# Kernel optimization log

Hardware: AMD Instinct MI355X
Metric: run time of the kernel (lower is better)

The kernel has to match this reference:

```python
import jax, jax.numpy as jnp
import numpy as np

SCALES = (1, 3, 6)
PRECISION = 10  # pywt default: 2**10 samples of psi on [-5, 5]


def _gaus1_filters():
    """Replicates pywt.cwt's integrated-wavelet filters for wavelet='gaus1'.

    pywt: psi, x = wavelet.wavefun(10); int_psi = cumsum(psi)*step; per scale a:
    j = arange(a*(x[-1]-x[0])+1)/(a*step) -> int indices; filter = int_psi[j][::-1];
    conv = np.convolve(data, filter). np.convolve flips its kernel, so the
    equivalent cross-correlation kernel (lax.conv semantics) is int_psi[j].
    """
    x = np.linspace(-5.0, 5.0, 2 ** PRECISION)
    step = x[1] - x[0]
    psi = -2.0 * x * np.exp(-x ** 2) / (np.pi / 2.0) ** 0.25
    int_psi = np.cumsum(psi) * step
    filts = []
    for a in SCALES:
        j = (np.arange(a * (x[-1] - x[0]) + 1) / (a * step)).astype(np.int64)
        j = j[j < int_psi.size]
        filts.append(int_psi[j].astype(np.float32))  # correlation kernel
    return filts

_FILTS = _gaus1_filters()


def setup_inputs() -> dict:
    key = jax.random.key(0)
    x = jax.random.normal(key, (32, 4096, 64), dtype=jnp.float32)
    return {"x": x}


def reference(x):
    B, S, C = x.shape
    sig = jnp.transpose(x, (0, 2, 1)).reshape(B * C, 1, S)  # [B*C, 1, S]
    outs = []
    for a, f in zip(SCALES, _FILTS):
        L = f.shape[0]
        k = jnp.asarray(f).reshape(1, 1, L)
        # full convolution (np.convolve): pad L-1 both sides
        conv = jax.lax.conv_general_dilated(
            sig, k, window_strides=(1,), padding=[(L - 1, L - 1)],
            dimension_numbers=("NCH", "OIH", "NCH"))  # [B*C, 1, S+L-1]
        coef = -np.sqrt(a).astype(np.float32) * jnp.diff(conv, axis=-1)  # [B*C,1,S+L-2]
        d = (coef.shape[-1] - S) / 2.0
        coef = coef[..., int(np.floor(d)): coef.shape[-1] - int(np.ceil(d))]  # [B*C,1,S]
        outs.append(coef)
    out = jnp.concatenate(outs, axis=1).reshape(B, C, len(SCALES), S)
    return jnp.transpose(out, (0, 2, 3, 1))  # [B, 3, S, C]
```

## Files before the change

### kernel.cpp

```cpp
#include <hip/hip_runtime.h>
#include <math.h>

#define S_LEN  4096
#define NCH    64
#define TILE_S 64
#define RPT    8
#define TY     8
#define NROWS  128
#define WLEN   70


constexpr double cexp_(double v) {
  const double LN2 = 0.6931471805599453;
  double t = v / LN2;
  int k = (int)t;
  if (t < 0.0 && (double)k != t) --k;
  double r = v - (double)k * LN2;
  double term = 1.0, sum = 1.0;
  for (int n = 1; n <= 22; ++n) { term *= r / (double)n; sum += term; }
  while (k > 0) { sum *= 2.0; --k; }
  while (k < 0) { sum *= 0.5; ++k; }
  return sum;
}
constexpr double csqrt_(double a) {
  double y = a > 1.0 ? a : 1.0;
  for (int i = 0; i < 64; ++i) y = 0.5 * (y + a / y);
  return y;
}
struct Wt { float w6[62]; float w3[32]; float w1[12]; };
constexpr Wt make_weights() {
  Wt w{};
  double ip[1024] = {};
  const double delta = 10.0 / 1023.0;
  const double step  = (-5.0 + delta) + 5.0;
  const double cn    = csqrt_(csqrt_(1.5707963267948966));
  double s = 0.0;
  for (int i = 0; i < 1024; ++i) {
    const double xi  = (i == 1023) ? 5.0 : ((double)i * delta - 5.0);
    const double psi = (-2.0 * xi) * cexp_(-(xi * xi)) / cn;
    s += psi;
    ip[i] = s * step;
  }
  const int as_[3] = {6, 3, 1};
  const int lf_[3] = {61, 31, 11};
  for (int si = 0; si < 3; ++si) {
    const double denom = (double)as_[si] * step;
    const float  sqa   = (float)csqrt_((double)as_[si]);
    const int    lf    = lf_[si];
    for (int t = 0; t <= lf; ++t) {
      float km1 = 0.f, kt = 0.f;
      if (t >= 1)      km1 = (float)ip[(long)(((double)(t - 1)) / denom)];
      if (t <= lf - 1) kt  = (float)ip[(long)(((double)t) / denom)];
      const float val = -sqa * (km1 - kt);
      if (si == 0) w.w6[t] = val; else if (si == 1) w.w3[t] = val; else w.w1[t] = val;
    }
  }
  return w;
}
constexpr Wt CW = make_weights();
template <int T> constexpr float W6 = CW.w6[T];
template <int T> constexpr float W3 = CW.w3[T];
template <int T> constexpr float W1 = CW.w1[T];

template <int K>
struct PreW {
  static __device__ __forceinline__ void run(const float* __restrict__ colbase,
                                             float (&win)[WLEN]) {
    win[K] = colbase[K * NCH];
    PreW<K + 1>::run(colbase, win);
  }
};
template <>
struct PreW<63> {
  static __device__ __forceinline__ void run(const float* __restrict__, float (&)[WLEN]) {}
};

template <int R, int T>
struct Tap {
  static __device__ __forceinline__ void run(const float (&win)[WLEN], float& a6,
                                             float& a3, float& a1) {
    a6 = fmaf(W6<T>, win[T + R + 1], a6);
    if constexpr (T >= 15 && T <= 46) a3 = fmaf(W3<T - 15>, win[T + R + 1], a3);
    if constexpr (T >= 25 && T <= 36) a1 = fmaf(W1<T - 25>, win[T + R + 1], a1);
    Tap<R, T + 1>::run(win, a6, a3, a1);
  }
};
template <int R>
struct Tap<R, 62> {
  static __device__ __forceinline__ void run(const float (&)[WLEN], float&, float&, float&) {}
};

template <int R>
struct Row {
  static __device__ __forceinline__ void run(const float* __restrict__ colbase,
                                             float (&win)[WLEN], float* __restrict__ o1,
                                             float* __restrict__ o3, float* __restrict__ o6) {
    if constexpr (R > 0) win[R + 62] = colbase[(R + 62) * NCH];
    float a6 = 0.f, a3 = 0.f, a1 = 0.f;
    Tap<R, 0>::run(win, a6, a3, a1);
    o1[(size_t)R * NCH] = a1;
    o3[(size_t)R * NCH] = a3;
    o6[(size_t)R * NCH] = a6;
    Row<R + 1>::run(colbase, win, o1, o3, o6);
  }
};
template <>
struct Row<RPT> {
  static __device__ __forceinline__ void run(const float* __restrict__, float (&)[WLEN],
                                             float* __restrict__, float* __restrict__,
                                             float* __restrict__) {}
};

__global__ __launch_bounds__(512, 6)
void cwt_main(const float* __restrict__ x, float* __restrict__ out) {
  __shared__ __align__(16) float lds[NROWS * NCH];

  const int c  = threadIdx.x;
  const int ty = threadIdx.y;
  const int tid = ty * 64 + c;

  const int hw = blockIdx.x;
  const int wg = ((hw & 7) << 8) + (hw >> 3);
  const int sx = wg & 63;
  const int b  = wg >> 6;
  const int s0 = sx * TILE_S;
  const int ROW0 = s0 - 32;

  const float* __restrict__ xb = x + (size_t)b * S_LEN * NCH;

  #pragma unroll
  for (int i = 0; i < 4; ++i) {
    const int slot = tid + i * 512;
    const int row  = slot >> 4, q = slot & 15;
    const int grow = ROW0 + row;
    float4 v = make_float4(0.f, 0.f, 0.f, 0.f);
    if ((unsigned)grow < (unsigned)S_LEN)
      v = *(const float4*)(xb + ((size_t)grow * NCH + (q << 2)));
    *(float4*)&lds[row * NCH + (q << 2)] = v;
  }
  __syncthreads();

  const float* __restrict__ colbase = &lds[(RPT * ty) * NCH + c];

  float win[WLEN];
  PreW<1>::run(colbase, win);

  const int srow = s0 + RPT * ty;
  float* o1 = out + (((size_t)b * 3 + 0) * S_LEN + srow) * NCH + c;
  float* o3 = out + (((size_t)b * 3 + 1) * S_LEN + srow) * NCH + c;
  float* o6 = out + (((size_t)b * 3 + 2) * S_LEN + srow) * NCH + c;

  Row<0>::run(colbase, win, o1, o3, o6);
}

extern "C" void kernel_launch(void* const* d_in, const int* in_sizes, int n_in,
                              void* d_out, int out_size, void* d_ws, size_t ws_size,
                              hipStream_t stream) {
  (void)n_in; (void)out_size; (void)d_ws; (void)ws_size;
  const float* x = (const float*)d_in[0];
  float* out = (float*)d_out;
  const int B = in_sizes[0] / (S_LEN * NCH);

  const int nblk = (S_LEN / TILE_S) * B;
  dim3 grid(nblk);
  dim3 block(NCH, TY);
  hipLaunchKernelGGL(cwt_main, grid, block, 0, stream, x, out);
}
```

Before: 136.1 us.

## Recast convolution as banded-Toeplitz MFMA with split-bf16 inputs

Replaces the per-thread scalar FMA sliding-window convolution with matrix-core MFMA 16x16x32 bf16 operations. The constant Toeplitz weight tiles are prebuilt in constant memory. Each input is split into high and low bf16 halves so two MFMAs roughly recover fp32 accuracy, and these are staged transposed per channel in XOR-swizzled LDS. The tile per block grows to 128 rows. This is meant to remove the large FMA instruction count, at the cost of bf16 weight rounding error, reduced occupancy and strided scalar global loads.

After: 133.4 us. 2.0% less time.

```diff
diff --git a/kernel.cpp b/kernel.cpp
--- a/kernel.cpp
+++ b/kernel.cpp
@@ -3,11 +3,14 @@
 
 #define S_LEN  4096
 #define NCH    64
-#define TILE_S 64
-#define RPT    8
+#define BTILE  128
 #define TY     8
-#define NROWS  128
-#define WLEN   70
+#define NCHUNK 26
+#define CSTR   256
+
+typedef __attribute__((ext_vector_type(8)))  short   short8v;
+typedef __attribute__((ext_vector_type(8)))  __bf16  bf16x8;
+typedef __attribute__((ext_vector_type(4)))  float   f32x4;
 
 
 constexpr double cexp_(double v) {
@@ -57,100 +60,123 @@
   }
   return w;
 }
-constexpr Wt CW = make_weights();
-template <int T> constexpr float W6 = CW.w6[T];
-template <int T> constexpr float W3 = CW.w3[T];
-template <int T> constexpr float W1 = CW.w1[T];
 
-template <int K>
-struct PreW {
-  static __device__ __forceinline__ void run(const float* __restrict__ colbase,
-                                             float (&win)[WLEN]) {
-    win[K] = colbase[K * NCH];
-    PreW<K + 1>::run(colbase, win);
-  }
-};
-template <>
-struct PreW<63> {
-  static __device__ __forceinline__ void run(const float* __restrict__, float (&)[WLEN]) {}
-};
+constexpr unsigned short bf16rne(float f) {
+  const unsigned u = __builtin_bit_cast(unsigned, f);
+  return (unsigned short)((u + 0x7FFFu + ((u >> 16) & 1u)) >> 16);
+}
 
-template <int R, int T>
-struct Tap {
-  static __device__ __forceinline__ void run(const float (&win)[WLEN], float& a6,
-                                             float& a3, float& a1) {
-    a6 = fmaf(W6<T>, win[T + R + 1], a6);
-    if constexpr (T >= 15 && T <= 46) a3 = fmaf(W3<T - 15>, win[T + R + 1], a3);
-    if constexpr (T >= 25 && T <= 36) a1 = fmaf(W1<T - 25>, win[T + R + 1], a1);
-    Tap<R, T + 1>::run(win, a6, a3, a1);
-  }
-};
-template <int R>
-struct Tap<R, 62> {
-  static __device__ __forceinline__ void run(const float (&)[WLEN], float&, float&, float&) {}
-};
+struct __align__(16) ATab { unsigned short v[6][64][8]; };
+constexpr ATab make_atab() {
+  ATab t{};
+  constexpr Wt w = make_weights();
+  for (int f = 0; f < 6; ++f)
+    for (int l = 0; l < 64; ++l)
+      for (int e = 0; e < 8; ++e) {
+        const int i = l & 15, k = (l >> 4) * 8 + e;
+        float val = 0.f;
+        if (f < 3)      { const int d = 32 * f + k - i - 1;       if (d >= 0 && d < 62) val = w.w6[d]; }
+        else if (f < 5) { const int d = 32 * (f - 3) + k - i;     if (d >= 0 && d < 32) val = w.w3[d]; }
+        else            { const int d = k - i - 2;                if (d >= 0 && d < 12) val = w.w1[d]; }
+        t.v[f][l][e] = bf16rne(val);
+      }
+  return t;
+}
+__constant__ ATab g_at = make_atab();
 
-template <int R>
-struct Row {
-  static __device__ __forceinline__ void run(const float* __restrict__ colbase,
-                                             float (&win)[WLEN], float* __restrict__ o1,
-                                             float* __restrict__ o3, float* __restrict__ o6) {
-    if constexpr (R > 0) win[R + 62] = colbase[(R + 62) * NCH];
-    float a6 = 0.f, a3 = 0.f, a1 = 0.f;
-    Tap<R, 0>::run(win, a6, a3, a1);
-    o1[(size_t)R * NCH] = a1;
-    o3[(size_t)R * NCH] = a3;
-    o6[(size_t)R * NCH] = a6;
-    Row<R + 1>::run(colbase, win, o1, o3, o6);
-  }
-};
-template <>
-struct Row<RPT> {
-  static __device__ __forceinline__ void run(const float* __restrict__, float (&)[WLEN],
-                                             float* __restrict__, float* __restrict__,
-                                             float* __restrict__) {}
-};
-
-__global__ __launch_bounds__(512, 6)
+__global__ __launch_bounds__(512, 4)
 void cwt_main(const float* __restrict__ x, float* __restrict__ out) {
-  __shared__ __align__(16) float lds[NROWS * NCH];
+  __shared__ __align__(16) unsigned short lds[2][NCH * CSTR];
 
   const int c  = threadIdx.x;
   const int ty = threadIdx.y;
-  const int tid = ty * 64 + c;
 
-  const int hw = blockIdx.x;
-  const int wg = ((hw & 7) << 8) + (hw >> 3);
-  const int sx = wg & 63;
-  const int b  = wg >> 6;
-  const int s0 = sx * TILE_S;
-  const int ROW0 = s0 - 32;
+  const int hw  = blockIdx.x;
+  const int npx = gridDim.x >> 3;
+  const int wg  = (hw & 7) * npx + (hw >> 3);
+  const int sg  = wg & ((S_LEN / BTILE) - 1);
+  const int b   = wg / (S_LEN / BTILE);
+  const int BS0 = sg * BTILE;
+  const int ROW0 = BS0 - 32;
 
   const float* __restrict__ xb = x + (size_t)b * S_LEN * NCH;
 
   #pragma unroll
-  for (int i = 0; i < 4; ++i) {
-    const int slot = tid + i * 512;
-    const int row  = slot >> 4, q = slot & 15;
-    const int grow = ROW0 + row;
-    float4 v = make_float4(0.f, 0.f, 0.f, 0.f);
-    if ((unsigned)grow < (unsigned)S_LEN)
-      v = *(const float4*)(xb + ((size_t)grow * NCH + (q << 2)));
-    *(float4*)&lds[row * NCH + (q << 2)] = v;
+  for (int q = 0; q < 4; ++q) {
+    const int cidx = ty + 8 * q;
+    if (cidx < NCHUNK) {
+      const int r0 = ROW0 + cidx * 8;
+      float v[8];
+      #pragma unroll
+      for (int r = 0; r < 8; ++r) {
+        const int row = r0 + r;
+        v[r] = ((unsigned)row < (unsigned)S_LEN) ? xb[(size_t)row * NCH + c] : 0.f;
+      }
+      short8v ph, pl;
+      #pragma unroll
+      for (int r = 0; r < 8; ++r) {
+        const unsigned u  = __builtin_bit_cast(unsigned, v[r]);
+        const unsigned h  = (u + 0x7FFFu + ((u >> 16) & 1u)) >> 16;
+        const float    fh = __builtin_bit_cast(float, h << 16);
+        const float    rl = v[r] - fh;
+        const unsigned ul = __builtin_bit_cast(unsigned, rl);
+        const unsigned lo = (ul + 0x7FFFu + ((ul >> 16) & 1u)) >> 16;
+        ph[r] = (short)h; pl[r] = (short)lo;
+      }
+      const int base = c * CSTR + ((cidx ^ (c & 7)) << 3);
+      *(short8v*)&lds[0][base] = ph;
+      *(short8v*)&lds[1][base] = pl;
+    }
   }
   __syncthreads();
 
-  const float* __restrict__ colbase = &lds[(RPT * ty) * NCH + c];
+  const int j  = c & 15;
+  const int ck = c >> 4;
+  const int hh = c & 7;
 
-  float win[WLEN];
-  PreW<1>::run(colbase, win);
+  const bf16x8 A60 = *(const bf16x8*)&g_at.v[0][c][0];
+  const bf16x8 A61 = *(const bf16x8*)&g_at.v[1][c][0];
+  const bf16x8 A62 = *(const bf16x8*)&g_at.v[2][c][0];
+  const bf16x8 A30 = *(const bf16x8*)&g_at.v[3][c][0];
+  const bf16x8 A31 = *(const bf16x8*)&g_at.v[4][c][0];
+  const bf16x8 A10 = *(const bf16x8*)&g_at.v[5][c][0];
 
-  const int srow = s0 + RPT * ty;
-  float* o1 = out + (((size_t)b * 3 + 0) * S_LEN + srow) * NCH + c;
-  float* o3 = out + (((size_t)b * 3 + 1) * S_LEN + srow) * NCH + c;
-  float* o6 = out + (((size_t)b * 3 + 2) * S_LEN + srow) * NCH + c;
+  const int cb0 = 2 * ty;
+  const size_t ob = (size_t)b * 3;
+  const int srow = BS0 + 16 * ty + ck * 4;
 
-  Row<0>::run(colbase, win, o1, o3, o6);
+  #pragma unroll
+  for (int jj = 0; jj < 4; ++jj) {
+    const int ch  = jj * 16 + j;
+    const int chb = ch * CSTR;
+    #define BRD(pl, cb) (*(const bf16x8*)&lds[pl][chb + ((((cb) + ck) ^ hh) << 3)])
+    f32x4 s6 = {0.f, 0.f, 0.f, 0.f};
+    f32x4 s3 = {0.f, 0.f, 0.f, 0.f};
+    f32x4 s1 = {0.f, 0.f, 0.f, 0.f};
+    s6 = __builtin_amdgcn_mfma_f32_16x16x32_bf16(A60, BRD(0, cb0 + 0), s6, 0, 0, 0);
+    s6 = __builtin_amdgcn_mfma_f32_16x16x32_bf16(A60, BRD(1, cb0 + 0), s6, 0, 0, 0);
+    s6 = __builtin_amdgcn_mfma_f32_16x16x32_bf16(A61, BRD(0, cb0 + 4), s6, 0, 0, 0);
+    s6 = __builtin_amdgcn_mfma_f32_16x16x32_bf16(A61, BRD(1, cb0 + 4), s6, 0, 0, 0);
+    s6 = __builtin_amdgcn_mfma_f32_16x16x32_bf16(A62, BRD(0, cb0 + 8), s6, 0, 0, 0);
+    s6 = __builtin_amdgcn_mfma_f32_16x16x32_bf16(A62, BRD(1, cb0 + 8), s6, 0, 0, 0);
+    s3 = __builtin_amdgcn_mfma_f32_16x16x32_bf16(A30, BRD(0, cb0 + 2), s3, 0, 0, 0);
+    s3 = __builtin_amdgcn_mfma_f32_16x16x32_bf16(A30, BRD(1, cb0 + 2), s3, 0, 0, 0);
+    s3 = __builtin_amdgcn_mfma_f32_16x16x32_bf16(A31, BRD(0, cb0 + 6), s3, 0, 0, 0);
+    s3 = __builtin_amdgcn_mfma_f32_16x16x32_bf16(A31, BRD(1, cb0 + 6), s3, 0, 0, 0);
+    s1 = __builtin_amdgcn_mfma_f32_16x16x32_bf16(A10, BRD(0, cb0 + 3), s1, 0, 0, 0);
+    s1 = __builtin_amdgcn_mfma_f32_16x16x32_bf16(A10, BRD(1, cb0 + 3), s1, 0, 0, 0);
+    #undef BRD
+
+    float* o1p = out + ((ob + 0) * S_LEN + srow) * NCH + ch;
+    float* o3p = out + ((ob + 1) * S_LEN + srow) * NCH + ch;
+    float* o6p = out + ((ob + 2) * S_LEN + srow) * NCH + ch;
+    #pragma unroll
+    for (int r = 0; r < 4; ++r) {
+      o1p[(size_t)r * NCH] = s1[r];
+      o3p[(size_t)r * NCH] = s3[r];
+      o6p[(size_t)r * NCH] = s6[r];
+    }
+  }
 }
 
 extern "C" void kernel_launch(void* const* d_in, const int* in_sizes, int n_in,
@@ -161,7 +187,7 @@
   float* out = (float*)d_out;
   const int B = in_sizes[0] / (S_LEN * NCH);
 
-  const int nblk = (S_LEN / TILE_S) * B;
+  const int nblk = (S_LEN / BTILE) * B;
   dim3 grid(nblk);
   dim3 block(NCH, TY);
   hipLaunchKernelGGL(cwt_main, grid, block, 0, stream, x, out);
```
